# Performance work log

Measured on AMD Instinct MI355X. Metric: run time of the kernel, lower is better.

## Reference

```python
import jax, jax.numpy as jnp
import numpy as np


def _reduce1(x):
    # x: [B, n, d] -> [B, 2d]; exists=max, forall=min over objects (exclude_self is a no-op for cnt=1)
    return jnp.concatenate([x.max(axis=1), x.min(axis=1)], axis=-1)


def _reduce2(x):
    # x: [B, n, n, d] -> [B, n, 2d]; exclude_self masks diagonal i==j (0 for exists/max, 1 for forall/min)
    n = x.shape[1]
    diag = jnp.eye(n, dtype=bool)[None, :, :, None]
    exists = jnp.where(diag, 0.0, x).max(axis=2)
    forall = jnp.where(diag, 1.0, x).min(axis=2)
    return jnp.concatenate([exists, forall], axis=-1)


def _layer(f0, f1, f2, p):
    # One LogicLayer step (breadth=2, minmax reducer, exclude_self, sigmoid norm, no hidden layers)
    W0, b0, W1, b1, W2, b2 = p
    B, n, d1 = f1.shape
    # order 0: [self, reduce(order1)]
    g0 = jnp.concatenate([f0, _reduce1(f1)], axis=-1)
    o0 = jax.nn.sigmoid(g0 @ W0 + b0)
    # order 1: [expand(order0), self, reduce(order2)]
    e0 = jnp.broadcast_to(f0[:, None, :], (B, n, f0.shape[-1]))
    g1 = jnp.concatenate([e0, f1, _reduce2(f2)], axis=-1)
    o1 = jax.nn.sigmoid(g1 @ W1 + b1)
    # order 2: [expand(order1), self] then Permutation(2) = cat(x, swap(i,j))
    e1 = jnp.broadcast_to(f1[:, :, None, :], (B, n, n, d1))
    g2 = jnp.concatenate([e1, f2], axis=-1)
    g2 = jnp.concatenate([g2, jnp.swapaxes(g2, 1, 2)], axis=-1)
    o2 = jax.nn.sigmoid(g2 @ W2 + b2)
    return o0, o1, o2


def setup_inputs() -> dict:
    key = jax.random.key(0)
    B, n = 4, 256
    d = [32, 64, 64]
    O = 128
    ks = iter(jax.random.split(key, 64))
    inp = {
        "x0": jax.random.uniform(next(ks), (B, d[0]), dtype=jnp.float32),
        "x1": jax.random.uniform(next(ks), (B, n, d[1]), dtype=jnp.float32),
        "x2": jax.random.uniform(next(ks), (B, n, n, d[2]), dtype=jnp.float32),
    }
    fan_ins = [
        (d[0] + 2 * d[1], d[0] + d[1] + 2 * d[2], 2 * (d[1] + d[2])),  # layer 0
        (O + 2 * O, O + O + 2 * O, 2 * (O + O)),                        # layer 1
        (O + 2 * O, O + O + 2 * O, 2 * (O + O)),                        # layer 2
    ]
    for l, fins in enumerate(fan_ins):
        for o, fin in enumerate(fins):
            inp[f"W{o}_{l}"] = jax.random.normal(next(ks), (fin, O), dtype=jnp.float32) / np.sqrt(fin).astype(np.float32)
            inp[f"b{o}_{l}"] = jnp.zeros((O,), dtype=jnp.float32)
    return inp


def reference(x0, x1, x2,
              W0_0, b0_0, W1_0, b1_0, W2_0, b2_0,
              W0_1, b0_1, W1_1, b1_1, W2_1, b2_1,
              W0_2, b0_2, W1_2, b1_2, W2_2, b2_2):
    f = (x0, x1, x2)
    for p in ((W0_0, b0_0, W1_0, b1_0, W2_0, b2_0),
              (W0_1, b0_1, W1_1, b1_1, W2_1, b2_1),
              (W0_2, b0_2, W1_2, b1_2, W2_2, b2_2)):
        f = _layer(*f, p)
    return f
```

## Files before the change

### kernel.cpp

```cpp
#include <hip/hip_runtime.h>
#include <hip/hip_bf16.h>
#include <cstdint>

#define NN 256
#define NB 4
#define OC 128

using bf16x8_t = __attribute__((ext_vector_type(8))) __bf16;
using f32x4_t  = __attribute__((ext_vector_type(4))) float;

typedef const __attribute__((address_space(1))) uint8_t* gptr1_t;
typedef __attribute__((address_space(3))) uint8_t* lptr3_t;

__device__ __forceinline__ void async_load16(const void* g, void* l) {
  __builtin_amdgcn_global_load_lds((gptr1_t)g, (lptr3_t)l, 16, 0, 0);
}

__device__ __forceinline__ float sigf(float x) {
  return 1.0f / (1.0f + __expf(-x));
}

__device__ __forceinline__ uint16_t f2bf_rne(float f) {
  uint32_t u = __float_as_uint(f);
  uint32_t r = (u + 0x7fffu + ((u >> 16) & 1u)) >> 16;
  return (uint16_t)r;
}

__device__ __forceinline__ void emit_wt(const float* __restrict__ W2,
                                        uint16_t* __restrict__ Wt, int d1,
                                        int d2, int idx) {
  const int K = 2 * d2;
  const int nn = idx / K, k = idx - nn * K;
  const int row = (k < d2) ? (d1 + k) : (2 * d1 + d2 + (k - d2));
  Wt[idx] = f2bf_rne(W2[row * OC + nn]);
}

__device__ __forceinline__ void emit_bt(const float* __restrict__ W1,
                                        const float* __restrict__ W2,
                                        uint16_t* __restrict__ Bt, int D0,
                                        int D1, int D2, int FIN1, int KP,
                                        int idx) {
  const int n = idx / KP, k = idx - n * KP;
  float val = 0.f;
  if (n < 128) {
    if (k < FIN1) val = W1[k * OC + n];
  } else if (n < 256) {
    if (k >= D0 && k < D0 + D1) val = W2[(k - D0) * OC + (n - 128)];
  } else {
    if (k >= D0 && k < D0 + D1) val = W2[(D1 + D2 + (k - D0)) * OC + (n - 256)];
  }
  Bt[idx] = f2bf_rne(val);
}

__global__ __launch_bounds__(256) void prep_all(
    const float* __restrict__ W2_0, const float* __restrict__ W2_1,
    const float* __restrict__ W2_2, const float* __restrict__ W1_0,
    const float* __restrict__ W1_1, const float* __restrict__ W1_2,
    uint16_t* __restrict__ Wt0, uint16_t* __restrict__ Wt1,
    uint16_t* __restrict__ Wt2, uint16_t* __restrict__ Bt0,
    uint16_t* __restrict__ Bt1, uint16_t* __restrict__ Bt2) {
  int g = blockIdx.x * 256 + threadIdx.x;
  if (g < 16384) { emit_wt(W2_0, Wt0, 64, 64, g); return; }
  g -= 16384;
  if (g < 32768) { emit_wt(W2_1, Wt1, 128, 128, g); return; }
  g -= 32768;
  if (g < 32768) { emit_wt(W2_2, Wt2, 128, 128, g); return; }
  g -= 32768;
  if (g < 98304) { emit_bt(W1_0, W2_0, Bt0, 32, 64, 64, 224, 256, g); return; }
  g -= 98304;
  if (g < 196608) { emit_bt(W1_1, W2_1, Bt1, 128, 128, 128, 512, 512, g); return; }
  g -= 196608;
  if (g < 196608) { emit_bt(W1_2, W2_2, Bt2, 128, 128, 128, 512, 512, g); }
}

__global__ __launch_bounds__(256) void reduce2_l0_kernel(
    const float* __restrict__ x2, const float* __restrict__ x0,
    const float* __restrict__ x1, uint16_t* __restrict__ g1bf0,
    uint16_t* __restrict__ x2bf, float* __restrict__ r2init) {
  const int bid = blockIdx.x;
  const int b = bid >> 8, i = bid & 255;
  const int tid = threadIdx.x;
  const int q = tid & 15, s = tid >> 4;
  const size_t rowbase = ((size_t)bid * NN) * 64 + q * 4;
  float mx0 = 0.f, mx1 = 0.f, mx2 = 0.f, mx3 = 0.f;
  float mn0 = 1.f, mn1 = 1.f, mn2 = 1.f, mn3 = 1.f;
  for (int j = s; j < NN; j += 16) {
    const float4 x = *(const float4*)(x2 + rowbase + (size_t)j * 64);
    uint2 pk;
    pk.x = (uint32_t)f2bf_rne(x.x) | ((uint32_t)f2bf_rne(x.y) << 16);
    pk.y = (uint32_t)f2bf_rne(x.z) | ((uint32_t)f2bf_rne(x.w) << 16);
    *(uint2*)(x2bf + rowbase + (size_t)j * 64) = pk;
    if (j != i) {
      mx0 = fmaxf(mx0, x.x); mx1 = fmaxf(mx1, x.y);
      mx2 = fmaxf(mx2, x.z); mx3 = fmaxf(mx3, x.w);
      mn0 = fminf(mn0, x.x); mn1 = fminf(mn1, x.y);
      mn2 = fminf(mn2, x.z); mn3 = fminf(mn3, x.w);
    }
  }
  __shared__ float4 smx[256], smn[256];
  smx[tid] = make_float4(mx0, mx1, mx2, mx3);
  smn[tid] = make_float4(mn0, mn1, mn2, mn3);
  __syncthreads();
  uint16_t* const g = g1bf0 + (size_t)bid * 256;
  if (s == 0) {
    for (int ss = 1; ss < 16; ++ss) {
      float4 a = smx[q + ss * 16], c = smn[q + ss * 16];
      mx0 = fmaxf(mx0, a.x); mx1 = fmaxf(mx1, a.y);
      mx2 = fmaxf(mx2, a.z); mx3 = fmaxf(mx3, a.w);
      mn0 = fminf(mn0, c.x); mn1 = fminf(mn1, c.y);
      mn2 = fminf(mn2, c.z); mn3 = fminf(mn3, c.w);
    }
    g[96 + q * 4 + 0] = f2bf_rne(mx0); g[96 + q * 4 + 1] = f2bf_rne(mx1);
    g[96 + q * 4 + 2] = f2bf_rne(mx2); g[96 + q * 4 + 3] = f2bf_rne(mx3);
    g[160 + q * 4 + 0] = f2bf_rne(mn0); g[160 + q * 4 + 1] = f2bf_rne(mn1);
    g[160 + q * 4 + 2] = f2bf_rne(mn2); g[160 + q * 4 + 3] = f2bf_rne(mn3);
  }
  if (tid < 32) g[tid] = f2bf_rne(x0[b * 32 + tid]);
  else if (tid < 96) g[tid] = f2bf_rne(x1[(size_t)bid * 64 + tid - 32]);
  else if (tid >= 224) g[tid] = 0;
  r2init[(size_t)bid * 256 + tid] = (tid < 128) ? 0.f : 1.f;
}

template <int D0, int D1, bool DUP>
__global__ __launch_bounds__(256) void o0_kernel(
    const float* __restrict__ f0, const float* __restrict__ f1,
    const float* __restrict__ W0, const float* __restrict__ b0,
    float* __restrict__ f0out, uint16_t* __restrict__ g1next) {
  constexpr int FIN = D0 + 2 * D1;
  constexpr int S = 256 / D1;
  const int b = blockIdx.x;
  const int tid = threadIdx.x;
  const int c = tid & (D1 - 1), s = tid / D1;
  __shared__ float g0[FIN];
  __shared__ float smx[256], smn[256];
  __shared__ float sval[128];
  float mx = -1e30f, mn = 1e30f;
  const float* f1b = f1 + (size_t)b * NN * D1;
  for (int j = s; j < NN; j += S) {
    float x = f1b[(size_t)j * D1 + c];
    mx = fmaxf(mx, x); mn = fminf(mn, x);
  }
  smx[tid] = mx; smn[tid] = mn;
  __syncthreads();
  if (s == 0) {
    for (int ss = 1; ss < S; ++ss) {
      mx = fmaxf(mx, smx[c + ss * D1]);
      mn = fminf(mn, smn[c + ss * D1]);
    }
    g0[D0 + c] = mx;
    g0[D0 + D1 + c] = mn;
  }
  if (tid < D0) g0[tid] = f0[b * D0 + tid];
  __syncthreads();
  if (tid < OC) {
    float acc = b0[tid];
#pragma unroll 8
    for (int k = 0; k < FIN; ++k) acc += g0[k] * W0[k * OC + tid];
    const float val = sigf(acc);
    f0out[b * OC + tid] = val;
    sval[tid] = val;
  }
  if (DUP) {
    __syncthreads();
    for (int idx = tid; idx < 256 * 128; idx += 256) {
      const int row = idx >> 7, cc = idx & 127;
      g1next[((size_t)(b * 256 + row)) * 512 + cc] = f2bf_rne(sval[cc]);
    }
  }
}

template <int KP, bool DUP>
__global__ __launch_bounds__(256) void small_gemm(
    const uint16_t* __restrict__ g1, const uint16_t* __restrict__ Bt,
    const float* __restrict__ b1, const float* __restrict__ b2,
    float* __restrict__ f1out, uint16_t* __restrict__ g1next,
    float* __restrict__ u, float* __restrict__ v) {
  constexpr int NCH = KP / 64;
  const int bid = blockIdx.x;
  const int mt = bid / 3, nt = bid - mt * 3;
  const int m0 = mt * 64, n0 = nt * 128;
  const int tid = threadIdx.x;
  const int wv = tid >> 6, lane = tid & 63;
  const int l15 = lane & 15, l4 = lane >> 4;

  __shared__ __align__(16) uint8_t ldsA[8192];
  __shared__ __align__(16) uint8_t ldsB[16384];

  f32x4_t acc[4][2];
#pragma unroll
  for (int a = 0; a < 4; ++a)
#pragma unroll
    for (int q = 0; q < 2; ++q) acc[a][q] = (f32x4_t){0.f, 0.f, 0.f, 0.f};

  for (int c = 0; c < NCH; ++c) {
    const int kbg = c * 64;
#pragma unroll
    for (int t = 0; t < 2; ++t) {
      const int id = wv * 2 + t;
      const int mi = id & 3, ks = id >> 2;
      async_load16(g1 + (size_t)(m0 + mi * 16 + l15) * KP + kbg + ks * 32 + l4 * 8,
                   ldsA + id * 1024);
    }
#pragma unroll
    for (int t = 0; t < 4; ++t) {
      const int id = wv * 4 + t;
      const int ni = id & 7, ks = id >> 3;
      async_load16(Bt + (size_t)(n0 + ni * 16 + l15) * KP + kbg + ks * 32 + l4 * 8,
                   ldsB + id * 1024);
    }
    __syncthreads();
#pragma unroll
    for (int ks = 0; ks < 2; ++ks) {
      bf16x8_t Af[4], Bf[2];
#pragma unroll
      for (int a = 0; a < 4; ++a)
        Af[a] = *(const bf16x8_t*)(ldsA + ((ks * 4 + a) << 10) + (lane << 4));
#pragma unroll
      for (int q = 0; q < 2; ++q)
        Bf[q] = *(const bf16x8_t*)(ldsB + ((ks * 8 + wv * 2 + q) << 10) + (lane << 4));
#pragma unroll
      for (int a = 0; a < 4; ++a)
#pragma unroll
        for (int q = 0; q < 2; ++q)
          acc[a][q] = __builtin_amdgcn_mfma_f32_16x16x32_bf16(Af[a], Bf[q],
                                                              acc[a][q], 0, 0, 0);
    }
    __syncthreads();
  }

  float bias[2];
#pragma unroll
  for (int q = 0; q < 2; ++q) {
    const int cc = wv * 32 + q * 16 + l15;
    bias[q] = (nt == 0) ? b1[cc] : ((nt == 1) ? b2[cc] : 0.f);
  }
#pragma unroll
  for (int a = 0; a < 4; ++a) {
    const int rl = a * 16 + l4 * 4;
#pragma unroll
    for (int r = 0; r < 4; ++r) {
      const size_t bi = m0 + rl + r;
#pragma unroll
      for (int q = 0; q < 2; ++q) {
        const int cc = wv * 32 + q * 16 + l15;
        const float x = acc[a][q][r] + bias[q];
        if (nt == 0) {
          const float val = sigf(x);
          f1out[bi * OC + cc] = val;
          if (DUP) g1next[bi * 512 + 128 + cc] = f2bf_rne(val);
        } else if (nt == 1) {
          u[bi * OC + cc] = x;
        } else {
          v[bi * OC + cc] = x;
        }
      }
    }
  }
}

template <bool INIT_NEXT>
__global__ __launch_bounds__(256) void conv_r2_kernel(
    const float* __restrict__ r2, uint16_t* __restrict__ g1next,
    float* __restrict__ r2next) {
  const int bi = blockIdx.x, t = threadIdx.x;
  g1next[(size_t)bi * 512 + 256 + t] = f2bf_rne(r2[(size_t)bi * 256 + t]);
  if (INIT_NEXT) r2next[(size_t)bi * 256 + t] = (t < 128) ? 0.f : 1.f;
}

template <int D2, typename OUT_T, bool REDUCE>
__global__ __launch_bounds__(256, 3) void gemm2_kernel(
    const __hip_bfloat16* __restrict__ f2, const uint16_t* __restrict__ Wt,
    const float* __restrict__ u, const float* __restrict__ v,
    OUT_T* __restrict__ out, float* __restrict__ r2n) {
  constexpr int K = 2 * D2;
  constexpr int NCH = K / 64;
  constexpr bool BF16OUT = (sizeof(OUT_T) == 2);
  constexpr int LDSB = BF16OUT ? (128 * 272) : 32768;
  const int bid = blockIdx.x;
  const int jt = bid & 1, i = (bid >> 1) & 255, b = bid >> 9;
  const int j0 = jt * 128;
  const int tid = threadIdx.x;
  const int wv = tid >> 6, lane = tid & 63;
  const int wr = wv >> 1, wc = wv & 1;
  const int l15 = lane & 15, l4 = lane >> 4;

  __shared__ __align__(16) uint8_t lds[LDSB];
  __shared__ unsigned smax[128], smin[128];
  uint8_t* const ldsA = lds;
  uint8_t* const ldsW = lds + 16384;

  const __hip_bfloat16* A1 = f2 + ((size_t)(b * NN + i) * NN + j0) * D2;
  const __hip_bfloat16* A2 = f2 + ((size_t)(b * NN + j0) * NN + i) * D2;

  f32x4_t acc[4][4];
#pragma unroll
  for (int a = 0; a < 4; ++a)
#pragma unroll
    for (int q = 0; q < 4; ++q) acc[a][q] = (f32x4_t){0.f, 0.f, 0.f, 0.f};

  for (int c = 0; c < NCH; ++c) {
    const int kbg = c * 64;
    const bool second = (kbg >= D2);
    const __hip_bfloat16* Ab = second ? A2 : A1;
    const size_t rstride = second ? (size_t)NN * D2 : (size_t)D2;
    const int kbase = second ? (kbg - D2) : kbg;
#pragma unroll
    for (int q = 0; q < 4; ++q) {
      const int id = wv * 4 + q;
      const int mi = id & 7, ks = id >> 3;
      const int row = mi * 16 + l15;
      const int kk = ks * 32 + l4 * 8;
      async_load16(Ab + (size_t)row * rstride + kbase + kk, ldsA + id * 1024);
    }
#pragma unroll
    for (int q = 0; q < 4; ++q) {
      const int id = wv * 4 + q;
      const int ni = id & 7, ks = id >> 3;
      const int nn2 = ni * 16 + l15;
      const int kk = ks * 32 + l4 * 8;
      async_load16(Wt + (size_t)nn2 * K + kbg + kk, ldsW + id * 1024);
    }
    __syncthreads();
#pragma unroll
    for (int ks = 0; ks < 2; ++ks) {
      bf16x8_t Af[4], Bf[4];
#pragma unroll
      for (int a = 0; a < 4; ++a)
        Af[a] = *(const bf16x8_t*)(ldsA + ((ks * 8 + wr * 4 + a) << 10) + (lane << 4));
#pragma unroll
      for (int q = 0; q < 4; ++q)
        Bf[q] = *(const bf16x8_t*)(ldsW + ((ks * 8 + wc * 4 + q) << 10) + (lane << 4));
#pragma unroll
      for (int a = 0; a < 4; ++a)
#pragma unroll
        for (int q = 0; q < 4; ++q)
          acc[a][q] = __builtin_amdgcn_mfma_f32_16x16x32_bf16(Af[a], Bf[q],
                                                              acc[a][q], 0, 0, 0);
    }
    __syncthreads();
  }

  const size_t bi2 = (size_t)(b * NN + i);
  float uval[4];
#pragma unroll
  for (int q = 0; q < 4; ++q) uval[q] = u[bi2 * OC + wc * 64 + q * 16 + l15];
  const size_t obase = (bi2 * NN + j0) * OC;
  const size_t vbase = (size_t)(b * NN + j0) * OC;

  if (BF16OUT) {
    if (REDUCE && tid < 128) { smax[tid] = 0u; smin[tid] = 0x3f800000u; }
    __syncthreads();
    float lmx[4] = {0.f, 0.f, 0.f, 0.f};
    float lmn[4] = {1.f, 1.f, 1.f, 1.f};
#pragma unroll
    for (int a = 0; a < 4; ++a) {
      const int rowb = wr * 64 + a * 16 + l4 * 4;
#pragma unroll
      for (int r = 0; r < 4; ++r) {
        const int j = rowb + r;
        const bool excl = (j0 + j) == i;
#pragma unroll
        for (int q = 0; q < 4; ++q) {
          const int col = wc * 64 + q * 16 + l15;
          const float x = acc[a][q][r] + uval[q] + v[vbase + (size_t)j * OC + col];
          const float sg = sigf(x);
          *(uint16_t*)(lds + j * 272 + col * 2) = f2bf_rne(sg);
          if (REDUCE && !excl) {
            lmx[q] = fmaxf(lmx[q], sg);
            lmn[q] = fminf(lmn[q], sg);
          }
        }
      }
    }
    if (REDUCE) {
#pragma unroll
      for (int q = 0; q < 4; ++q) {
        const int col = wc * 64 + q * 16 + l15;
        atomicMax(&smax[col], __float_as_uint(lmx[q]));
        atomicMin(&smin[col], __float_as_uint(lmn[q]));
      }
    }
    __syncthreads();
    uint16_t* const outp = (uint16_t*)out;
#pragma unroll
    for (int ci = 0; ci < 8; ++ci) {
      const int chunk = ci * 256 + tid;
      const int row = chunk >> 4, off = chunk & 15;
      const uint4 val = *(const uint4*)(lds + row * 272 + off * 16);
      *(uint4*)(outp + obase + (size_t)row * OC + off * 8) = val;
    }
    if (REDUCE && tid < 128) {
      unsigned* const r2u = (unsigned*)r2n;
      atomicMax(&r2u[bi2 * 256 + tid], smax[tid]);
      atomicMin(&r2u[bi2 * 256 + 128 + tid], smin[tid]);
    }
  } else {
    float* const outp = (float*)out;
#pragma unroll
    for (int a = 0; a < 4; ++a) {
      const int rowb = wr * 64 + a * 16 + l4 * 4;
#pragma unroll
      for (int r = 0; r < 4; ++r) {
        const int j = rowb + r;
#pragma unroll
        for (int q = 0; q < 4; ++q) {
          const int col = wc * 64 + q * 16 + l15;
          const float x = acc[a][q][r] + uval[q] + v[vbase + (size_t)j * OC + col];
          outp[obase + (size_t)j * OC + col] = sigf(x);
        }
      }
    }
  }
}

extern "C" void kernel_launch(void* const* d_in, const int* in_sizes, int n_in,
                              void* d_out, int out_size, void* d_ws,
                              size_t ws_size, hipStream_t stream) {
  const float* x0 = (const float*)d_in[0];
  const float* x1 = (const float*)d_in[1];
  const float* x2 = (const float*)d_in[2];
  const float *Wp[3][3], *bp[3][3];
  for (int l = 0; l < 3; ++l)
    for (int o = 0; o < 3; ++o) {
      Wp[l][o] = (const float*)d_in[3 + l * 6 + o * 2];
      bp[l][o] = (const float*)d_in[3 + l * 6 + o * 2 + 1];
    }

  const size_t F2E = (size_t)NB * NN * NN * OC;
  const size_t X2E = (size_t)NB * NN * NN * 64;

  uint8_t* ws = (uint8_t*)d_ws;
  size_t off = 0;
  auto carve = [&](size_t bytes) -> uint8_t* {
    uint8_t* p = ws + off;
    off += (bytes + 255) & ~(size_t)255;
    return p;
  };
  float* f0a = (float*)carve((size_t)NB * OC * 4);
  float* f0b = (float*)carve((size_t)NB * OC * 4);
  float* f1a = (float*)carve((size_t)NB * NN * OC * 4);
  float* f1b = (float*)carve((size_t)NB * NN * OC * 4);
  float* r2b = (float*)carve((size_t)NB * NN * 256 * 4);
  float* r2c = (float*)carve((size_t)NB * NN * 256 * 4);
  float* uu  = (float*)carve((size_t)NB * NN * OC * 4);
  float* vv  = (float*)carve((size_t)NB * NN * OC * 4);
  uint16_t* Wt0 = (uint16_t*)carve((size_t)OC * 128 * 2);
  uint16_t* Wt1 = (uint16_t*)carve((size_t)OC * 256 * 2);
  uint16_t* Wt2 = (uint16_t*)carve((size_t)OC * 256 * 2);
  uint16_t* Bt0 = (uint16_t*)carve((size_t)384 * 256 * 2);
  uint16_t* Bt1 = (uint16_t*)carve((size_t)384 * 512 * 2);
  uint16_t* Bt2 = (uint16_t*)carve((size_t)384 * 512 * 2);
  uint16_t* g1bf0 = (uint16_t*)carve((size_t)NB * NN * 256 * 2);
  uint16_t* g1bf1 = (uint16_t*)carve((size_t)NB * NN * 512 * 2);
  uint16_t* g1bf2 = (uint16_t*)carve((size_t)NB * NN * 512 * 2);
  __hip_bfloat16* f2a = (__hip_bfloat16*)carve(F2E * 2);

  __hip_bfloat16* f2b;
  uint16_t* x2bf;
  if (ws_size >= off + F2E * 2) {
    f2b = (__hip_bfloat16*)carve(F2E * 2);
    x2bf = (uint16_t*)f2b;
  } else {
    f2b = (__hip_bfloat16*)d_in[2];
    x2bf = (uint16_t*)carve(X2E * 2);
  }

  float* out_f0 = (float*)d_out;
  float* out_f1 = out_f0 + (size_t)NB * OC;
  float* out_f2 = out_f1 + (size_t)NB * NN * OC;

  prep_all<<<2240, 256, 0, stream>>>(Wp[0][2], Wp[1][2], Wp[2][2], Wp[0][1],
                                     Wp[1][1], Wp[2][1], Wt0, Wt1, Wt2, Bt0,
                                     Bt1, Bt2);
  reduce2_l0_kernel<<<NB * NN, 256, 0, stream>>>(x2, x0, x1, g1bf0, x2bf, r2b);

  o0_kernel<32, 64, true><<<NB, 256, 0, stream>>>(x0, x1, Wp[0][0], bp[0][0],
                                                  f0a, g1bf1);
  small_gemm<256, true><<<48, 256, 0, stream>>>(g1bf0, Bt0, bp[0][1], bp[0][2],
                                                f1a, g1bf1, uu, vv);
  gemm2_kernel<64, __hip_bfloat16, true><<<NB * NN * 2, 256, 0, stream>>>(
      (const __hip_bfloat16*)x2bf, Wt0, uu, vv, f2a, r2b);
  conv_r2_kernel<true><<<NB * NN, 256, 0, stream>>>(r2b, g1bf1, r2c);

  o0_kernel<128, 128, true><<<NB, 256, 0, stream>>>(f0a, f1a, Wp[1][0],
                                                    bp[1][0], f0b, g1bf2);
  small_gemm<512, true><<<48, 256, 0, stream>>>(g1bf1, Bt1, bp[1][1], bp[1][2],
                                                f1b, g1bf2, uu, vv);
  gemm2_kernel<128, __hip_bfloat16, true><<<NB * NN * 2, 256, 0, stream>>>(
      f2a, Wt1, uu, vv, f2b, r2c);
  conv_r2_kernel<false><<<NB * NN, 256, 0, stream>>>(r2c, g1bf2, nullptr);

  o0_kernel<128, 128, false><<<NB, 256, 0, stream>>>(f0b, f1b, Wp[2][0],
                                                     bp[2][0], out_f0, nullptr);
  small_gemm<512, false><<<48, 256, 0, stream>>>(g1bf2, Bt2, bp[2][1], bp[2][2],
                                                 out_f1, nullptr, uu, vv);
  gemm2_kernel<128, float, false><<<NB * NN * 2, 256, 0, stream>>>(
      f2b, Wt2, uu, vv, out_f2, nullptr);
}
```

Baseline: 539.7 us.

## Merge small kernels: fuse o0 into small_gemm, r2 conversion into gemm2 epilogue

```diff
diff --git a/kernel.cpp b/kernel.cpp
--- a/kernel.cpp
+++ b/kernel.cpp
@@ -36,10 +36,9 @@
 }
 
 __device__ __forceinline__ void emit_bt(const float* __restrict__ W1,
-                                        const float* __restrict__ W2,
-                                        uint16_t* __restrict__ Bt, int D0,
-                                        int D1, int D2, int FIN1, int KP,
-                                        int idx) {
+                                        const float* __restrict__ W2, uint16_t* __restrict__ Bt,
+                                        int D0, int D1, int D2, int FIN1,
+                                        int KP, int idx) {
   const int n = idx / KP, k = idx - n * KP;
   float val = 0.f;
   if (n < 128) {
@@ -56,9 +55,12 @@
     const float* __restrict__ W2_0, const float* __restrict__ W2_1,
     const float* __restrict__ W2_2, const float* __restrict__ W1_0,
     const float* __restrict__ W1_1, const float* __restrict__ W1_2,
+    const float* __restrict__ x0, const float* __restrict__ x1,
     uint16_t* __restrict__ Wt0, uint16_t* __restrict__ Wt1,
     uint16_t* __restrict__ Wt2, uint16_t* __restrict__ Bt0,
-    uint16_t* __restrict__ Bt1, uint16_t* __restrict__ Bt2) {
+    uint16_t* __restrict__ Bt1, uint16_t* __restrict__ Bt2,
+    uint16_t* __restrict__ g1bf0, float* __restrict__ r2b,
+    float* __restrict__ r2c, unsigned* __restrict__ cnt) {
   int g = blockIdx.x * 256 + threadIdx.x;
   if (g < 16384) { emit_wt(W2_0, Wt0, 64, 64, g); return; }
   g -= 16384;
@@ -70,38 +72,69 @@
   g -= 98304;
   if (g < 196608) { emit_bt(W1_1, W2_1, Bt1, 128, 128, 128, 512, 512, g); return; }
   g -= 196608;
-  if (g < 196608) { emit_bt(W1_2, W2_2, Bt2, 128, 128, 128, 512, 512, g); }
+  if (g < 196608) { emit_bt(W1_2, W2_2, Bt2, 128, 128, 128, 512, 512, g); return; }
+  g -= 196608;
+  if (g < 131072) {
+    const int row = g >> 7, t = g & 127;
+    uint16_t* const gp = g1bf0 + (size_t)row * 256;
+    if (t < 32) gp[t] = f2bf_rne(x0[(row >> 8) * 32 + t]);
+    else if (t < 96) gp[t] = f2bf_rne(x1[(size_t)row * 64 + (t - 32)]);
+    else gp[128 + t] = 0;
+    return;
+  }
+  g -= 131072;
+  if (g < 262144) { r2b[g] = ((g & 255) < 128) ? 0.f : 1.f; return; }
+  g -= 262144;
+  if (g < 262144) { r2c[g] = ((g & 255) < 128) ? 0.f : 1.f; return; }
+  g -= 262144;
+  if (g < 2048) cnt[g] = 0u;
 }
 
 __global__ __launch_bounds__(256) void reduce2_l0_kernel(
-    const float* __restrict__ x2, const float* __restrict__ x0,
-    const float* __restrict__ x1, uint16_t* __restrict__ g1bf0,
-    uint16_t* __restrict__ x2bf, float* __restrict__ r2init) {
+    const float* __restrict__ x2, uint16_t* __restrict__ g1bf0,
+    uint16_t* __restrict__ x2bf) {
   const int bid = blockIdx.x;
-  const int b = bid >> 8, i = bid & 255;
+  const int i = bid & 255;
   const int tid = threadIdx.x;
   const int q = tid & 15, s = tid >> 4;
   const size_t rowbase = ((size_t)bid * NN) * 64 + q * 4;
-  float mx0 = 0.f, mx1 = 0.f, mx2 = 0.f, mx3 = 0.f;
-  float mn0 = 1.f, mn1 = 1.f, mn2 = 1.f, mn3 = 1.f;
-  for (int j = s; j < NN; j += 16) {
-    const float4 x = *(const float4*)(x2 + rowbase + (size_t)j * 64);
-    uint2 pk;
-    pk.x = (uint32_t)f2bf_rne(x.x) | ((uint32_t)f2bf_rne(x.y) << 16);
-    pk.y = (uint32_t)f2bf_rne(x.z) | ((uint32_t)f2bf_rne(x.w) << 16);
-    *(uint2*)(x2bf + rowbase + (size_t)j * 64) = pk;
-    if (j != i) {
-      mx0 = fmaxf(mx0, x.x); mx1 = fmaxf(mx1, x.y);
-      mx2 = fmaxf(mx2, x.z); mx3 = fmaxf(mx3, x.w);
-      mn0 = fminf(mn0, x.x); mn1 = fminf(mn1, x.y);
-      mn2 = fminf(mn2, x.z); mn3 = fminf(mn3, x.w);
-    }
-  }
+  float mxA0 = 0.f, mxA1 = 0.f, mxA2 = 0.f, mxA3 = 0.f;
+  float mnA0 = 1.f, mnA1 = 1.f, mnA2 = 1.f, mnA3 = 1.f;
+  float mxB0 = 0.f, mxB1 = 0.f, mxB2 = 0.f, mxB3 = 0.f;
+  float mnB0 = 1.f, mnB1 = 1.f, mnB2 = 1.f, mnB3 = 1.f;
+#pragma unroll 2
+  for (int t = 0; t < 16; t += 2) {
+    const int jA = s + t * 16, jB = jA + 16;
+    const float4 xa = *(const float4*)(x2 + rowbase + (size_t)jA * 64);
+    const float4 xb = *(const float4*)(x2 + rowbase + (size_t)jB * 64);
+    uint2 pa, pb;
+    pa.x = (uint32_t)f2bf_rne(xa.x) | ((uint32_t)f2bf_rne(xa.y) << 16);
+    pa.y = (uint32_t)f2bf_rne(xa.z) | ((uint32_t)f2bf_rne(xa.w) << 16);
+    pb.x = (uint32_t)f2bf_rne(xb.x) | ((uint32_t)f2bf_rne(xb.y) << 16);
+    pb.y = (uint32_t)f2bf_rne(xb.z) | ((uint32_t)f2bf_rne(xb.w) << 16);
+    *(uint2*)(x2bf + rowbase + (size_t)jA * 64) = pa;
+    *(uint2*)(x2bf + rowbase + (size_t)jB * 64) = pb;
+    if (jA != i) {
+      mxA0 = fmaxf(mxA0, xa.x); mxA1 = fmaxf(mxA1, xa.y);
+      mxA2 = fmaxf(mxA2, xa.z); mxA3 = fmaxf(mxA3, xa.w);
+      mnA0 = fminf(mnA0, xa.x); mnA1 = fminf(mnA1, xa.y);
+      mnA2 = fminf(mnA2, xa.z); mnA3 = fminf(mnA3, xa.w);
+    }
+    if (jB != i) {
+      mxB0 = fmaxf(mxB0, xb.x); mxB1 = fmaxf(mxB1, xb.y);
+      mxB2 = fmaxf(mxB2, xb.z); mxB3 = fmaxf(mxB3, xb.w);
+      mnB0 = fminf(mnB0, xb.x); mnB1 = fminf(mnB1, xb.y);
+      mnB2 = fminf(mnB2, xb.z); mnB3 = fminf(mnB3, xb.w);
+    }
+  }
+  float mx0 = fmaxf(mxA0, mxB0), mx1 = fmaxf(mxA1, mxB1);
+  float mx2 = fmaxf(mxA2, mxB2), mx3 = fmaxf(mxA3, mxB3);
+  float mn0 = fminf(mnA0, mnB0), mn1 = fminf(mnA1, mnB1);
+  float mn2 = fminf(mnA2, mnB2), mn3 = fminf(mnA3, mnB3);
   __shared__ float4 smx[256], smn[256];
   smx[tid] = make_float4(mx0, mx1, mx2, mx3);
   smn[tid] = make_float4(mn0, mn1, mn2, mn3);
   __syncthreads();
-  uint16_t* const g = g1bf0 + (size_t)bid * 256;
   if (s == 0) {
     for (int ss = 1; ss < 16; ++ss) {
       float4 a = smx[q + ss * 16], c = smn[q + ss * 16];
@@ -110,168 +143,158 @@
       mn0 = fminf(mn0, c.x); mn1 = fminf(mn1, c.y);
       mn2 = fminf(mn2, c.z); mn3 = fminf(mn3, c.w);
     }
+    uint16_t* const g = g1bf0 + (size_t)bid * 256;
     g[96 + q * 4 + 0] = f2bf_rne(mx0); g[96 + q * 4 + 1] = f2bf_rne(mx1);
     g[96 + q * 4 + 2] = f2bf_rne(mx2); g[96 + q * 4 + 3] = f2bf_rne(mx3);
     g[160 + q * 4 + 0] = f2bf_rne(mn0); g[160 + q * 4 + 1] = f2bf_rne(mn1);
     g[160 + q * 4 + 2] = f2bf_rne(mn2); g[160 + q * 4 + 3] = f2bf_rne(mn3);
   }
-  if (tid < 32) g[tid] = f2bf_rne(x0[b * 32 + tid]);
-  else if (tid < 96) g[tid] = f2bf_rne(x1[(size_t)bid * 64 + tid - 32]);
-  else if (tid >= 224) g[tid] = 0;
-  r2init[(size_t)bid * 256 + tid] = (tid < 128) ? 0.f : 1.f;
-}
-
-template <int D0, int D1, bool DUP>
-__global__ __launch_bounds__(256) void o0_kernel(
-    const float* __restrict__ f0, const float* __restrict__ f1,
-    const float* __restrict__ W0, const float* __restrict__ b0,
-    float* __restrict__ f0out, uint16_t* __restrict__ g1next) {
-  constexpr int FIN = D0 + 2 * D1;
-  constexpr int S = 256 / D1;
-  const int b = blockIdx.x;
-  const int tid = threadIdx.x;
-  const int c = tid & (D1 - 1), s = tid / D1;
-  __shared__ float g0[FIN];
-  __shared__ float smx[256], smn[256];
-  __shared__ float sval[128];
-  float mx = -1e30f, mn = 1e30f;
-  const float* f1b = f1 + (size_t)b * NN * D1;
-  for (int j = s; j < NN; j += S) {
-    float x = f1b[(size_t)j * D1 + c];
-    mx = fmaxf(mx, x); mn = fminf(mn, x);
-  }
-  smx[tid] = mx; smn[tid] = mn;
-  __syncthreads();
-  if (s == 0) {
-    for (int ss = 1; ss < S; ++ss) {
-      mx = fmaxf(mx, smx[c + ss * D1]);
-      mn = fminf(mn, smn[c + ss * D1]);
-    }
-    g0[D0 + c] = mx;
-    g0[D0 + D1 + c] = mn;
-  }
-  if (tid < D0) g0[tid] = f0[b * D0 + tid];
-  __syncthreads();
-  if (tid < OC) {
-    float acc = b0[tid];
-#pragma unroll 8
-    for (int k = 0; k < FIN; ++k) acc += g0[k] * W0[k * OC + tid];
-    const float val = sigf(acc);
-    f0out[b * OC + tid] = val;
-    sval[tid] = val;
-  }
-  if (DUP) {
-    __syncthreads();
-    for (int idx = tid; idx < 256 * 128; idx += 256) {
-      const int row = idx >> 7, cc = idx & 127;
-      g1next[((size_t)(b * 256 + row)) * 512 + cc] = f2bf_rne(sval[cc]);
-    }
-  }
-}
-
-template <int KP, bool DUP>
+}
+
+template <int KP, int D0, int D1, bool DUP>
 __global__ __launch_bounds__(256) void small_gemm(
     const uint16_t* __restrict__ g1, const uint16_t* __restrict__ Bt,
     const float* __restrict__ b1, const float* __restrict__ b2,
     float* __restrict__ f1out, uint16_t* __restrict__ g1next,
-    float* __restrict__ u, float* __restrict__ v) {
+    float* __restrict__ u, float* __restrict__ v,
+    const float* __restrict__ f0in, const float* __restrict__ f1in,
+    const float* __restrict__ W0, const float* __restrict__ b0,
+    float* __restrict__ f0out) {
   constexpr int NCH = KP / 64;
   const int bid = blockIdx.x;
-  const int mt = bid / 3, nt = bid - mt * 3;
-  const int m0 = mt * 64, n0 = nt * 128;
   const int tid = threadIdx.x;
-  const int wv = tid >> 6, lane = tid & 63;
-  const int l15 = lane & 15, l4 = lane >> 4;
 
   __shared__ __align__(16) uint8_t ldsA[8192];
   __shared__ __align__(16) uint8_t ldsB[16384];
 
-  f32x4_t acc[4][2];
-#pragma unroll
-  for (int a = 0; a < 4; ++a)
-#pragma unroll
-    for (int q = 0; q < 2; ++q) acc[a][q] = (f32x4_t){0.f, 0.f, 0.f, 0.f};
-
-  for (int c = 0; c < NCH; ++c) {
-    const int kbg = c * 64;
-#pragma unroll
-    for (int t = 0; t < 2; ++t) {
-      const int id = wv * 2 + t;
-      const int mi = id & 3, ks = id >> 2;
-      async_load16(g1 + (size_t)(m0 + mi * 16 + l15) * KP + kbg + ks * 32 + l4 * 8,
-                   ldsA + id * 1024);
-    }
-#pragma unroll
-    for (int t = 0; t < 4; ++t) {
-      const int id = wv * 4 + t;
-      const int ni = id & 7, ks = id >> 3;
-      async_load16(Bt + (size_t)(n0 + ni * 16 + l15) * KP + kbg + ks * 32 + l4 * 8,
-                   ldsB + id * 1024);
-    }
+  if (bid < 48) {
+    const int mt = bid / 3, nt = bid - mt * 3;
+    const int m0 = mt * 64, n0 = nt * 128;
+    const int wv = tid >> 6, lane = tid & 63;
+    const int l15 = lane & 15, l4 = lane >> 4;
+
+    f32x4_t acc[4][2];
+#pragma unroll
+    for (int a = 0; a < 4; ++a)
+#pragma unroll
+      for (int q = 0; q < 2; ++q) acc[a][q] = (f32x4_t){0.f, 0.f, 0.f, 0.f};
+
+    for (int c = 0; c < NCH; ++c) {
+      const int kbg = c * 64;
+#pragma unroll
+      for (int t = 0; t < 2; ++t) {
+        const int id = wv * 2 + t;
+        const int mi = id & 3, ks = id >> 2;
+        async_load16(g1 + (size_t)(m0 + mi * 16 + l15) * KP + kbg + ks * 32 + l4 * 8,
+                     ldsA + id * 1024);
+      }
+#pragma unroll
+      for (int t = 0; t < 4; ++t) {
+        const int id = wv * 4 + t;
+        const int ni = id & 7, ks = id >> 3;
+        async_load16(Bt + (size_t)(n0 + ni * 16 + l15) * KP + kbg + ks * 32 + l4 * 8,
+                     ldsB + id * 1024);
+      }
+      __syncthreads();
+#pragma unroll
+      for (int ks = 0; ks < 2; ++ks) {
+        bf16x8_t Af[4], Bf[2];
+#pragma unroll
+        for (int a = 0; a < 4; ++a)
+          Af[a] = *(const bf16x8_t*)(ldsA + ((ks * 4 + a) << 10) + (lane << 4));
+#pragma unroll
+        for (int q = 0; q < 2; ++q)
+          Bf[q] = *(const bf16x8_t*)(ldsB + ((ks * 8 + wv * 2 + q) << 10) + (lane << 4));
+#pragma unroll
+        for (int a = 0; a < 4; ++a)
+#pragma unroll
+          for (int q = 0; q < 2; ++q)
+            acc[a][q] = __builtin_amdgcn_mfma_f32_16x16x32_bf16(Af[a], Bf[q],
+                                                                acc[a][q], 0, 0, 0);
+      }
+      __syncthreads();
+    }
+
+    float bias[2];
+#pragma unroll
+    for (int q = 0; q < 2; ++q) {
+      const int cc = wv * 32 + q * 16 + l15;
+      bias[q] = (nt == 0) ? b1[cc] : ((nt == 1) ? b2[cc] : 0.f);
+    }
+#pragma unroll
+    for (int a = 0; a < 4; ++a) {
+      const int rl = a * 16 + l4 * 4;
+#pragma unroll
+      for (int r = 0; r < 4; ++r) {
+        const size_t bi = m0 + rl + r;
+#pragma unroll
+        for (int q = 0; q < 2; ++q) {
+          const int cc = wv * 32 + q * 16 + l15;
+          const float x = acc[a][q][r] + bias[q];
+          if (nt == 0) {
+            const float val = sigf(x);
+            f1out[bi * OC + cc] = val;
+            if (DUP) g1next[bi * 512 + 128 + cc] = f2bf_rne(val);
+          } else if (nt == 1) {
+            u[bi * OC + cc] = x;
+          } else {
+            v[bi * OC + cc] = x;
+          }
+        }
+      }
+    }
+  } else {
+    constexpr int FIN0 = D0 + 2 * D1;
+    constexpr int S = 256 / D1;
+    const int b = bid - 48;
+    float* const sm = (float*)ldsA;
+    float* const g0 = sm;
+    float* const smx = sm + 512;
+    float* const smn = sm + 768;
+    float* const sval = sm + 1024;
+    const int cc = tid & (D1 - 1), ss = tid / D1;
+    float mx = -1e30f, mn = 1e30f;
+    const float* f1b = f1in + (size_t)b * NN * D1;
+    for (int j = ss; j < NN; j += S) {
+      const float x = f1b[(size_t)j * D1 + cc];
+      mx = fmaxf(mx, x); mn = fminf(mn, x);
+    }
+    smx[tid] = mx; smn[tid] = mn;
     __syncthreads();
-#pragma unroll
-    for (int ks = 0; ks < 2; ++ks) {
-      bf16x8_t Af[4], Bf[2];
-#pragma unroll
-      for (int a = 0; a < 4; ++a)
-        Af[a] = *(const bf16x8_t*)(ldsA + ((ks * 4 + a) << 10) + (lane << 4));
-#pragma unroll
-      for (int q = 0; q < 2; ++q)
-        Bf[q] = *(const bf16x8_t*)(ldsB + ((ks * 8 + wv * 2 + q) << 10) + (lane << 4));
-#pragma unroll
-      for (int a = 0; a < 4; ++a)
-#pragma unroll
-        for (int q = 0; q < 2; ++q)
-          acc[a][q] = __builtin_amdgcn_mfma_f32_16x16x32_bf16(Af[a], Bf[q],
-                                                              acc[a][q], 0, 0, 0);
-    }
+    if (ss == 0) {
+      for (int s2 = 1; s2 < S; ++s2) {
+        mx = fmaxf(mx, smx[cc + s2 * D1]);
+        mn = fminf(mn, smn[cc + s2 * D1]);
+      }
+      g0[D0 + cc] = mx;
+      g0[D0 + D1 + cc] = mn;
+    }
+    if (tid < D0) g0[tid] = f0in[b * D0 + tid];
     __syncthreads();
-  }
-
-  float bias[2];
-#pragma unroll
-  for (int q = 0; q < 2; ++q) {
-    const int cc = wv * 32 + q * 16 + l15;
-    bias[q] = (nt == 0) ? b1[cc] : ((nt == 1) ? b2[cc] : 0.f);
-  }
-#pragma unroll
-  for (int a = 0; a < 4; ++a) {
-    const int rl = a * 16 + l4 * 4;
-#pragma unroll
-    for (int r = 0; r < 4; ++r) {
-      const size_t bi = m0 + rl + r;
-#pragma unroll
-      for (int q = 0; q < 2; ++q) {
-        const int cc = wv * 32 + q * 16 + l15;
-        const float x = acc[a][q][r] + bias[q];
-        if (nt == 0) {
-          const float val = sigf(x);
-          f1out[bi * OC + cc] = val;
-          if (DUP) g1next[bi * 512 + 128 + cc] = f2bf_rne(val);
-        } else if (nt == 1) {
-          u[bi * OC + cc] = x;
-        } else {
-          v[bi * OC + cc] = x;
-        }
-      }
-    }
-  }
-}
-
-template <bool INIT_NEXT>
-__global__ __launch_bounds__(256) void conv_r2_kernel(
-    const float* __restrict__ r2, uint16_t* __restrict__ g1next,
-    float* __restrict__ r2next) {
-  const int bi = blockIdx.x, t = threadIdx.x;
-  g1next[(size_t)bi * 512 + 256 + t] = f2bf_rne(r2[(size_t)bi * 256 + t]);
-  if (INIT_NEXT) r2next[(size_t)bi * 256 + t] = (t < 128) ? 0.f : 1.f;
+    if (tid < OC) {
+      float acc = b0[tid];
+#pragma unroll 8
+      for (int k = 0; k < FIN0; ++k) acc += g0[k] * W0[k * OC + tid];
+      const float val = sigf(acc);
+      f0out[b * OC + tid] = val;
+      sval[tid] = val;
+    }
+    if (DUP) {
+      __syncthreads();
+      for (int idx = tid; idx < 256 * 128; idx += 256) {
+        const int row = idx >> 7, c2 = idx & 127;
+        g1next[((size_t)(b * 256 + row)) * 512 + c2] = f2bf_rne(sval[c2]);
+      }
+    }
+  }
 }
 
 template <int D2, typename OUT_T, bool REDUCE>
 __global__ __launch_bounds__(256, 3) void gemm2_kernel(
     const __hip_bfloat16* __restrict__ f2, const uint16_t* __restrict__ Wt,
     const float* __restrict__ u, const float* __restrict__ v,
-    OUT_T* __restrict__ out, float* __restrict__ r2n) {
+    OUT_T* __restrict__ out, float* __restrict__ r2n,
+    unsigned* __restrict__ cnt, uint16_t* __restrict__ g1next) {
   constexpr int K = 2 * D2;
   constexpr int NCH = K / 64;
   constexpr bool BF16OUT = (sizeof(OUT_T) == 2);
@@ -286,6 +309,7 @@
 
   __shared__ __align__(16) uint8_t lds[LDSB];
   __shared__ unsigned smax[128], smin[128];
+  __shared__ unsigned sflag;
   uint8_t* const ldsA = lds;
   uint8_t* const ldsW = lds + 16384;
 
@@ -389,10 +413,22 @@
       const uint4 val = *(const uint4*)(lds + row * 272 + off * 16);
       *(uint4*)(outp + obase + (size_t)row * OC + off * 8) = val;
     }
-    if (REDUCE && tid < 128) {
+    if (REDUCE) {
       unsigned* const r2u = (unsigned*)r2n;
-      atomicMax(&r2u[bi2 * 256 + tid], smax[tid]);
-      atomicMin(&r2u[bi2 * 256 + 128 + tid], smin[tid]);
+      if (tid < 128) {
+        atomicMax(&r2u[bi2 * 256 + tid], smax[tid]);
+        atomicMin(&r2u[bi2 * 256 + 128 + tid], smin[tid]);
+      }
+      __syncthreads();
+      if (tid == 0) {
+        __threadfence();
+        sflag = (atomicAdd(&cnt[bi2], 1u) == 1u) ? 1u : 0u;
+      }
+      __syncthreads();
+      if (sflag) {
+        const unsigned uv2 = atomicOr(&r2u[bi2 * 256 + tid], 0u);
+        g1next[bi2 * 512 + 256 + tid] = f2bf_rne(__uint_as_float(uv2));
+      }
     }
   } else {
     float* const outp = (float*)out;
@@ -444,6 +480,9 @@
   float* r2c = (float*)carve((size_t)NB * NN * 256 * 4);
   float* uu  = (float*)carve((size_t)NB * NN * OC * 4);
   float* vv  = (float*)carve((size_t)NB * NN * OC * 4);
+  unsigned* cnt = (unsigned*)carve((size_t)2 * NB * NN * 4);
+  unsigned* cnt1 = cnt;
+  unsigned* cnt2 = cnt + NB * NN;
   uint16_t* Wt0 = (uint16_t*)carve((size_t)OC * 128 * 2);
   uint16_t* Wt1 = (uint16_t*)carve((size_t)OC * 256 * 2);
   uint16_t* Wt2 = (uint16_t*)carve((size_t)OC * 256 * 2);
@@ -469,31 +508,26 @@
   float* out_f1 = out_f0 + (size_t)NB * OC;
   float* out_f2 = out_f1 + (size_t)NB * NN * OC;
 
-  prep_all<<<2240, 256, 0, stream>>>(Wp[0][2], Wp[1][2], Wp[2][2], Wp[0][1],
-                                     Wp[1][1], Wp[2][1], Wt0, Wt1, Wt2, Bt0,
-                                     Bt1, Bt2);
-  reduce2_l0_kernel<<<NB * NN, 256, 0, stream>>>(x2, x0, x1, g1bf0, x2bf, r2b);
-
-  o0_kernel<32, 64, true><<<NB, 256, 0, stream>>>(x0, x1, Wp[0][0], bp[0][0],
-                                                  f0a, g1bf1);
-  small_gemm<256, true><<<48, 256, 0, stream>>>(g1bf0, Bt0, bp[0][1], bp[0][2],
-                                                f1a, g1bf1, uu, vv);
+  prep_all<<<4808, 256, 0, stream>>>(Wp[0][2], Wp[1][2], Wp[2][2], Wp[0][1],
+                                     Wp[1][1], Wp[2][1], x0, x1, Wt0, Wt1, Wt2,
+                                     Bt0, Bt1, Bt2, g1bf0, r2b, r2c, cnt);
+  reduce2_l0_kernel<<<NB * NN, 256, 0, stream>>>(x2, g1bf0, x2bf);
+
+  small_gemm<256, 32, 64, true><<<52, 256, 0, stream>>>(
+      g1bf0, Bt0, bp[0][1], bp[0][2], f1a, g1bf1, uu, vv, x0, x1, Wp[0][0],
+      bp[0][0], f0a);
   gemm2_kernel<64, __hip_bfloat16, true><<<NB * NN * 2, 256, 0, stream>>>(
-      (const __hip_bfloat16*)x2bf, Wt0, uu, vv, f2a, r2b);
-  conv_r2_kernel<true><<<NB * NN, 256, 0, stream>>>(r2b, g1bf1, r2c);
-
-  o0_kernel<128, 128, true><<<NB, 256, 0, stream>>>(f0a, f1a, Wp[1][0],
-                                                    bp[1][0], f0b, g1bf2);
-  small_gemm<512, true><<<48, 256, 0, stream>>>(g1bf1, Bt1, bp[1][1], bp[1][2],
-                                                f1b, g1bf2, uu, vv);
+      (const __hip_bfloat16*)x2bf, Wt0, uu, vv, f2a, r2b, cnt1, g1bf1);
+
+  small_gemm<512, 128, 128, true><<<52, 256, 0, stream>>>(
+      g1bf1, Bt1, bp[1][1], bp[1][2], f1b, g1bf2, uu, vv, f0a, f1a, Wp[1][0],
+      bp[1][0], f0b);
   gemm2_kernel<128, __hip_bfloat16, true><<<NB * NN * 2, 256, 0, stream>>>(
-      f2a, Wt1, uu, vv, f2b, r2c);
-  conv_r2_kernel<false><<<NB * NN, 256, 0, stream>>>(r2c, g1bf2, nullptr);
-
-  o0_kernel<128, 128, false><<<NB, 256, 0, stream>>>(f0b, f1b, Wp[2][0],
-                                                     bp[2][0], out_f0, nullptr);
-  small_gemm<512, false><<<48, 256, 0, stream>>>(g1bf2, Bt2, bp[2][1], bp[2][2],
-                                                 out_f1, nullptr, uu, vv);
+      f2a, Wt1, uu, vv, f2b, r2c, cnt2, g1bf2);
+
+  small_gemm<512, 128, 128, false><<<52, 256, 0, stream>>>(
+      g1bf2, Bt2, bp[2][1], bp[2][2], out_f1, nullptr, uu, vv, f0b, f1b,
+      Wp[2][0], bp[2][0], out_f0);
   gemm2_kernel<128, float, false><<<NB * NN * 2, 256, 0, stream>>>(
-      f2b, Wt2, uu, vv, out_f2, nullptr);
-}
+      f2b, Wt2, uu, vv, out_f2, nullptr, nullptr, nullptr);
+}
```

Result: slower. 627.9 us (+16.3%).
